# Performance work log

Hardware: AMD Instinct MI355X
Metric: run time of the kernel (lower is better)

The kernel has to match this reference:

```python
import jax, jax.numpy as jnp
import numpy as np

QDEPTH = 20
WIDTH = HEIGHT = 28
PIXELS = WIDTH * HEIGHT          # 784
WIRES = 10                        # ceil(log2(784))
BATCH = 8192


def setup_inputs() -> dict:
    key = jax.random.key(0)
    k1, k2, k3, k4 = jax.random.split(key, 4)
    x = jax.random.normal(k1, (BATCH, 1, WIDTH, HEIGHT), jnp.float32)
    W = jax.random.normal(k2, (WIRES, PIXELS), jnp.float32) / np.sqrt(PIXELS)
    b = jax.random.normal(k3, (WIRES,), jnp.float32) * 0.01
    qweights = jax.random.normal(k4, (QDEPTH, WIRES, 3), jnp.float32) * 0.4
    return {"x": x, "W": W, "b": b, "qweights": qweights}


def _apply_1q(state, gate, wire):
    """Apply a single-qubit gate. state: (B,)+(2,)*WIRES; gate: (2,2) or (B,2,2)."""
    ax = 1 + wire
    s = jnp.moveaxis(state, ax, 1)
    shp = s.shape
    s = s.reshape(shp[0], 2, -1)
    if gate.ndim == 2:
        s = jnp.einsum('ij,bjr->bir', gate, s)
    else:
        s = jnp.einsum('bij,bjr->bir', gate, s)
    return jnp.moveaxis(s.reshape(shp), 1, ax)


def _cnot(state, c, t):
    """CNOT with control c, target t on state (B,)+(2,)*WIRES."""
    s = jnp.moveaxis(state, (1 + c, 1 + t), (1, 2))
    # when control==1, flip target axis
    s = jnp.concatenate([s[:, :1], jnp.flip(s[:, 1:2], axis=2)], axis=1)
    return jnp.moveaxis(s, (1, 2), (1 + c, 1 + t))


def _ry_batched(theta):
    """theta: (B,) -> (B,2,2) complex RY gates."""
    c = jnp.cos(theta / 2)
    s = jnp.sin(theta / 2)
    g = jnp.stack([jnp.stack([c, -s], -1), jnp.stack([s, c], -1)], -2)
    return g.astype(jnp.complex64)


def _rot(phi, theta, omega):
    """PennyLane Rot(phi,theta,omega) = RZ(omega) RY(theta) RZ(phi), scalars -> (2,2)."""
    c = jnp.cos(theta / 2)
    s = jnp.sin(theta / 2)
    m00 = jnp.exp(-0.5j * (phi + omega)) * c
    m01 = -jnp.exp(0.5j * (phi - omega)) * s
    m10 = jnp.exp(-0.5j * (phi - omega)) * s
    m11 = jnp.exp(0.5j * (phi + omega)) * c
    return jnp.stack([jnp.stack([m00, m01]), jnp.stack([m10, m11])]).astype(jnp.complex64)


def _forward(x, W, b, qweights):
    B = x.shape[0]
    feat = x.reshape(B, -1)                       # b 1 w h -> b (w h)
    angles = feat @ W.T + b                       # linear_down -> (B, WIRES)

    # |0...0> statevector, wire 0 most significant (PennyLane convention)
    state = jnp.zeros((B,) + (2,) * WIRES, jnp.complex64)
    state = state.at[(slice(None),) + (0,) * WIRES].set(1.0)

    # AngleEmbedding, rotation='Y'
    for w in range(WIRES):
        state = _apply_1q(state, _ry_batched(angles[:, w]), w)

    # StronglyEntanglingLayers: per-layer Rot on every wire, then CNOT ring
    for l in range(QDEPTH):
        for w in range(WIRES):
            state = _apply_1q(state, _rot(qweights[l, w, 0], qweights[l, w, 1], qweights[l, w, 2]), w)
        r = (l % (WIRES - 1)) + 1                 # default PennyLane ranges
        for w in range(WIRES):
            state = _cnot(state, w, (w + r) % WIRES)

    sv = state.reshape(B, -1)
    probs = sv.real ** 2 + sv.imag ** 2           # qml.probs over all wires
    out = jnp.clip(probs[:, :PIXELS] * PIXELS, 0.0, 1.0)
    return out.reshape(B, 1, WIDTH, HEIGHT)


def reference(x, W, b, qweights):
    return _forward(x, W, b, qweights)
```

## Files before the change

kernel.cpp:

```cpp
#include <hip/hip_runtime.h>
#include <hip/hip_bf16.h>
#include <stdint.h>


#define NWIRES  10
#define DIM     1024
#define NLAYERS 20
#define NGATES  200
#define NPASS   100
#define PIXELS  784
#define BATCH   8192

typedef _Float16 f16;
typedef _Float16 f16x8 __attribute__((ext_vector_type(8)));
typedef float    f32x4 __attribute__((ext_vector_type(4)));
typedef float    f32x2 __attribute__((ext_vector_type(2)));

typedef const __attribute__((address_space(1))) void* gas1_t;
typedef __attribute__((address_space(3))) void*       las3_t;

__device__ __forceinline__ void gload_lds16(const void* g, void* l) {
  __builtin_amdgcn_global_load_lds((gas1_t)g, (las3_t)l, 16, 0, 0);
}

__global__ __launch_bounds__(256) void k_prep(const float* __restrict__ qw,
                                              float* __restrict__ plan_mat,
                                              unsigned* __restrict__ plan_idx,
                                              unsigned* __restrict__ plan_final,
                                              unsigned* __restrict__ jtab) {
  __shared__ float    gm[NGATES][8];
  __shared__ unsigned shb[NPASS * 8];
  __shared__ unsigned shr[NPASS * 8];
  __shared__ unsigned pp[NPASS][4];
  const int tid = threadIdx.x;

  if (tid < NGATES) {
    float phi = qw[tid * 3 + 0], th = qw[tid * 3 + 1], om = qw[tid * 3 + 2];
    float s, c, sa, ca, sb, cb;
    sincosf(0.5f * th, &s, &c);
    sincosf(0.5f * (phi + om), &sa, &ca);
    sincosf(0.5f * (phi - om), &sb, &cb);
    gm[tid][0] = ca * c;  gm[tid][1] = sa * c;
    gm[tid][2] = cb * s;  gm[tid][3] = sb * s;
    gm[tid][4] = -cb * s; gm[tid][5] = sb * s;
    gm[tid][6] = ca * c;  gm[tid][7] = -sa * c;
  }
  __syncthreads();

  if (tid == 0) {
    unsigned rA[NWIRES], ic[NWIRES];
#pragma unroll
    for (int i = 0; i < NWIRES; i++) { rA[i] = 1u << i; ic[i] = 1u << i; }
#pragma unroll
    for (int lrev = 0; lrev < NLAYERS; lrev++) {
      const int l = NLAYERS - 1 - lrev;
      const int r = (l % (NWIRES - 1)) + 1;
#pragma unroll
      for (int w = NWIRES - 1; w >= 0; w--) {
        const int t = (w + r) % NWIRES;
        rA[9 - t] ^= rA[9 - w];
        ic[9 - w] ^= ic[9 - t];
      }
#pragma unroll
      for (int s = 0; s < 5; s++) {
        const int p1 = 9 - 2 * s, p2 = 8 - 2 * s;
        unsigned u1 = rA[p1], u2 = rA[p2];
        unsigned m1 = ic[p1], m2 = ic[p2];
        unsigned b1 = u1 & (0u - u1);
        if (u2 & b1) u2 ^= u1;
        unsigned b2 = u2 & (0u - u2);
        if (u1 & b2) u1 ^= u2;
        const int pid = lrev * 5 + s;
        pp[pid][0] = u1; pp[pid][1] = u2;
        pp[pid][2] = b1; pp[pid][3] = b2;
        plan_idx[pid * 8 + 6] = m1;
        plan_idx[pid * 8 + 7] = m2;
      }
    }
#pragma unroll
    for (int p = 0; p < NWIRES; p++) plan_final[p] = ic[p];
  } else if (tid >= 100 && tid < 200) {
    int t = tid - 100;
    int lrev = t / 5, s = t % 5;
    int l = NLAYERS - 1 - lrev;
    int g1 = l * NWIRES + 2 * s, g2 = g1 + 1;
    float* K = plan_mat + (size_t)t * 64;
#pragma unroll
    for (int r = 0; r < 4; r++) {
#pragma unroll
      for (int c = 0; c < 4; c++) {
        int r1 = r >> 1, c1 = c >> 1, r2 = r & 1, c2 = c & 1;
        float ar = gm[g1][(r1 * 2 + c1) * 2], ai = gm[g1][(r1 * 2 + c1) * 2 + 1];
        float br = gm[g2][(r2 * 2 + c2) * 2], bi = gm[g2][(r2 * 2 + c2) * 2 + 1];
        float kr = ar * br - ai * bi;
        float ki = ar * bi + ai * br;
        float* e = K + (r * 4 + c) * 4;
        e[0] = kr; e[1] = kr; e[2] = -ki; e[3] = ki;
      }
    }
  }
  __syncthreads();

  if (tid < NPASS) {
    const int pid = tid;
    const unsigned u1 = pp[pid][0], u2 = pp[pid][1];
    const unsigned b1 = pp[pid][2], b2 = pp[pid][3];
    unsigned echPack = 0;
    int cnt = 0, nrem = 0;
    for (int f = 0; f < NWIRES; f++) {
      unsigned ef = 1u << f;
      if (ef == b1 || ef == b2) continue;
      unsigned v = ef ^ (((u1 >> f) & 1u) ? b1 : 0u)
                      ^ (((u2 >> f) & 1u) ? b2 : 0u);
      unsigned n = v & 15u;
#pragma unroll
      for (int rep = 0; rep < 4; rep++) {
#pragma unroll
        for (int k2 = 0; k2 < 4; k2++) {
          unsigned h = (echPack >> (8 * k2)) & 255u;
          if (h) {
            unsigned hb = 0x80000000u >> __clz(h);
            if (n & hb) n ^= h;
          }
        }
      }
      if (n && cnt < 4) {
        echPack |= n << (8 * cnt);
        shb[pid * 8 + cnt] = v;
        cnt++;
      } else {
        shr[pid * 8 + nrem] = v;
        nrem++;
      }
    }
    for (int i = 0; i < nrem; i++) shb[pid * 8 + cnt + i] = shr[pid * 8 + i];
  }
  __syncthreads();

  for (int t = 0; t < NPASS; t++) {
    unsigned j = 0;
#pragma unroll
    for (int b = 0; b < 8; b++)
      if ((tid >> b) & 1) j ^= shb[t * 8 + b];
    jtab[t * 256 + tid] = j;
  }
}

__global__ __launch_bounds__(256) void k_main(const float* __restrict__ plan_mat,
                                              const unsigned* __restrict__ plan_idx,
                                              const unsigned* __restrict__ plan_final,
                                              const unsigned* __restrict__ jtab,
                                              const float* __restrict__ x,
                                              const float* __restrict__ W,
                                              const float* __restrict__ bias,
                                              f16* __restrict__ E,
                                              f16* __restrict__ Bt) {
  __shared__ f32x2 st[DIM];
  __shared__ float part[4][NWIRES];
  __shared__ float csh[NWIRES][2];

  const int tid = threadIdx.x;

  if (blockIdx.x < PIXELS) {
    const int col = blockIdx.x;

    for (int i = tid; i < DIM; i += 256)
      st[i] = (f32x2){i == col ? 1.f : 0.f, 0.f};

    unsigned jn = jtab[tid];
    __syncthreads();

    for (int t = 0; t < NPASS; t++) {
      const unsigned* P = plan_idx + (size_t)t * 8;
      const unsigned m1 = P[6], m2 = P[7];
      const f32x4* Kp = (const f32x4*)(plan_mat + (size_t)t * 64);

      const unsigned j = jn;
      if (t + 1 < NPASS) jn = jtab[(t + 1) * 256 + tid];

      f32x2 v0 = st[j];
      f32x2 v1 = st[j ^ m2];
      f32x2 v2 = st[j ^ m1];
      f32x2 v3 = st[j ^ m1 ^ m2];
      f32x2 w0 = {v0.y, v0.x}, w1 = {v1.y, v1.x};
      f32x2 w2 = {v2.y, v2.x}, w3 = {v3.y, v3.x};

      f32x2 r0 = {0.f, 0.f}, r1 = {0.f, 0.f}, r2 = {0.f, 0.f}, r3 = {0.f, 0.f};
#define CM(rr, e, vv, ww)                         \
      { f32x4 kk = Kp[e];                         \
        rr += (f32x2){kk.x, kk.y} * (vv);         \
        rr += (f32x2){kk.z, kk.w} * (ww); }
      CM(r0, 0, v0, w0)  CM(r0, 1, v1, w1)  CM(r0, 2, v2, w2)  CM(r0, 3, v3, w3)
      CM(r1, 4, v0, w0)  CM(r1, 5, v1, w1)  CM(r1, 6, v2, w2)  CM(r1, 7, v3, w3)
      CM(r2, 8, v0, w0)  CM(r2, 9, v1, w1)  CM(r2, 10, v2, w2) CM(r2, 11, v3, w3)
      CM(r3, 12, v0, w0) CM(r3, 13, v1, w1) CM(r3, 14, v2, w2) CM(r3, 15, v3, w3)
#undef CM

      st[j]           = r0;
      st[j ^ m2]      = r1;
      st[j ^ m1]      = r2;
      st[j ^ m1 ^ m2] = r3;
      __syncthreads();
    }

    unsigned invl[NWIRES];
#pragma unroll
    for (int p = 0; p < NWIRES; p++) invl[p] = plan_final[p];

    __align__(8) f16 re4[4], im4[4];
#pragma unroll
    for (int u = 0; u < 4; u++) {
      int i = tid * 4 + u;
      unsigned j = 0;
#pragma unroll
      for (int p = 0; p < NWIRES; p++)
        if ((i >> p) & 1) j ^= invl[p];
      f32x2 v = st[j];
      re4[u] = (f16)v.x;
      im4[u] = (f16)(-v.y);
    }
    *(uint2*)(&Bt[(size_t)(2 * col) * DIM + tid * 4])     = *(const uint2*)re4;
    *(uint2*)(&Bt[(size_t)(2 * col + 1) * DIM + tid * 4]) = *(const uint2*)im4;
    return;
  }

  const int b = blockIdx.x - PIXELS;
  const float* xr = x + (size_t)b * PIXELS;

  float acc[NWIRES];
#pragma unroll
  for (int w = 0; w < NWIRES; w++) acc[w] = 0.f;

  for (int k = tid; k < PIXELS; k += 256) {
    float xv = xr[k];
#pragma unroll
    for (int w = 0; w < NWIRES; w++) acc[w] = fmaf(xv, W[w * PIXELS + k], acc[w]);
  }

#pragma unroll
  for (int w = 0; w < NWIRES; w++) {
    float v = acc[w];
#pragma unroll
    for (int off = 32; off > 0; off >>= 1) v += __shfl_xor(v, off, 64);
    acc[w] = v;
  }

  const int wv = tid >> 6, ln = tid & 63;
  if (ln == 0) {
#pragma unroll
    for (int w = 0; w < NWIRES; w++) part[wv][w] = acc[w];
  }
  __syncthreads();
  if (tid < NWIRES) {
    float a = part[0][tid] + part[1][tid] + part[2][tid] + part[3][tid] + bias[tid];
    float s, c;
    sincosf(0.5f * a, &s, &c);
    csh[tid][0] = c;
    csh[tid][1] = s;
  }
  __syncthreads();

  __align__(8) f16 e4[4];
#pragma unroll
  for (int u = 0; u < 4; u++) {
    int i = tid * 4 + u;
    float pr = 1.f;
#pragma unroll
    for (int w = 0; w < NWIRES; w++) pr *= csh[w][(i >> (9 - w)) & 1];
    e4[u] = (f16)pr;
  }
  *(uint2*)(&E[(size_t)b * DIM + tid * 4]) = *(const uint2*)e4;
}

__global__ __launch_bounds__(256, 2) void k_gemm(const f16* __restrict__ E,
                                                 const f16* __restrict__ Bt,
                                                 float* __restrict__ out) {
  __shared__ __align__(16) f16 As[4][128 * 32];
  __shared__ __align__(16) f16 Bs[4][128 * 32];

  const int tid = threadIdx.x;
  const int wid = tid >> 6, ln = tid & 63;
  const int wm = wid >> 1, wn = wid & 1;

  const int bid = blockIdx.x;
  const int swz = (bid & 7) * 104 + (bid >> 3);
  const int mt  = swz % 64, nt = swz / 64;
  const int m0  = mt * 128;
  const int n0  = nt * 128;

  f32x4 acc[4][4];
#pragma unroll
  for (int a = 0; a < 4; a++)
#pragma unroll
    for (int q = 0; q < 4; q++) acc[a][q] = (f32x4){0.f, 0.f, 0.f, 0.f};

  int offA[4], offB[4];
#pragma unroll
  for (int mi = 0; mi < 4; mi++) {
    int Ra = wm * 64 + mi * 16 + (ln & 15);
    offA[mi] = Ra * 32 + (((ln >> 4) ^ ((Ra >> 1) & 3)) * 8);
  }
#pragma unroll
  for (int ni = 0; ni < 4; ni++) {
    int Rb = wn * 64 + ni * 16 + (ln & 15);
    offB[ni] = Rb * 32 + (((ln >> 4) ^ ((Rb >> 1) & 3)) * 8);
  }

  auto stage = [&](int t) {
    const int sb = t & 3;
#pragma unroll
    for (int r = 0; r < 2; r++) {
      int u   = r * 256 + tid;
      int row = u >> 2;
      int c16 = (u & 3) ^ ((row >> 1) & 3);
      gload_lds16((const char*)E + (size_t)(m0 + row) * 2048 + t * 64 + c16 * 16,
                  (char*)&As[sb][0] + (size_t)u * 16);
    }
#pragma unroll
    for (int r = 0; r < 2; r++) {
      int u   = r * 256 + tid;
      int row = u >> 2;
      int c16 = (u & 3) ^ ((row >> 1) & 3);
      gload_lds16((const char*)Bt + (size_t)(n0 + row) * 2048 + t * 64 + c16 * 16,
                  (char*)&Bs[sb][0] + (size_t)u * 16);
    }
  };

  stage(0);
  stage(1);
  stage(2);
  asm volatile("s_waitcnt vmcnt(8)" ::: "memory");
  __builtin_amdgcn_s_barrier();

#pragma unroll 4
  for (int k = 0; k < 32; k++) {
    const int buf = k & 3;
    f16x8 af[4], bf[4];
#pragma unroll
    for (int mi = 0; mi < 4; mi++) af[mi] = *(const f16x8*)&As[buf][offA[mi]];
#pragma unroll
    for (int ni = 0; ni < 4; ni++) bf[ni] = *(const f16x8*)&Bs[buf][offB[ni]];

    if (k < 29) stage(k + 3);

    __builtin_amdgcn_s_setprio(1);
#pragma unroll
    for (int mi = 0; mi < 4; mi++)
#pragma unroll
      for (int ni = 0; ni < 4; ni++)
        acc[mi][ni] = __builtin_amdgcn_mfma_f32_16x16x32_f16(
            af[mi], bf[ni], acc[mi][ni], 0, 0, 0);
    __builtin_amdgcn_s_setprio(0);

    if (k < 29)       { asm volatile("s_waitcnt vmcnt(8)" ::: "memory"); }
    else if (k == 29) { asm volatile("s_waitcnt vmcnt(4)" ::: "memory"); }
    else if (k == 30) { asm volatile("s_waitcnt vmcnt(0)" ::: "memory"); }
    __builtin_amdgcn_s_barrier();
  }

#pragma unroll
  for (int mi = 0; mi < 4; mi++) {
#pragma unroll
    for (int ni = 0; ni < 4; ni++) {
      int n = n0 + wn * 64 + ni * 16 + (ln & 15);
      int p = n >> 1;
      bool even = (ln & 1) == 0;
#pragma unroll
      for (int r = 0; r < 4; r++) {
        float v = acc[mi][ni][r];
        float o = __shfl_xor(v, 1, 64);
        if (even && p < PIXELS) {
          int m = m0 + wm * 64 + mi * 16 + (ln >> 4) * 4 + r;
          float s2 = (v * v + o * o) * (float)PIXELS;
          out[(size_t)m * PIXELS + p] = fminf(fmaxf(s2, 0.f), 1.f);
        }
      }
    }
  }
}

extern "C" void kernel_launch(void* const* d_in, const int* in_sizes, int n_in,
                              void* d_out, int out_size, void* d_ws, size_t ws_size,
                              hipStream_t stream) {
  const float* x    = (const float*)d_in[0];
  const float* W    = (const float*)d_in[1];
  const float* bias = (const float*)d_in[2];
  const float* qw   = (const float*)d_in[3];
  float* out        = (float*)d_out;

  char* ws = (char*)d_ws;
  f16* E  = (f16*)(ws);
  f16* Bt = (f16*)(ws + (size_t)16 * 1024 * 1024);
  float*    plan_mat   = (float*)(ws + (size_t)20 * 1024 * 1024);
  unsigned* plan_idx   = (unsigned*)(ws + (size_t)20 * 1024 * 1024 + 65536);
  unsigned* plan_final = (unsigned*)(ws + (size_t)20 * 1024 * 1024 + 131072);
  unsigned* jtab       = (unsigned*)(ws + (size_t)20 * 1024 * 1024 + 196608);

  k_prep<<<dim3(1), dim3(256), 0, stream>>>(qw, plan_mat, plan_idx, plan_final,
                                            jtab);
  k_main<<<dim3(PIXELS + BATCH), dim3(256), 0, stream>>>(plan_mat, plan_idx,
                                                         plan_final, jtab,
                                                         x, W, bias, E, Bt);
  k_gemm<<<dim3(832), dim3(256), 0, stream>>>(E, Bt, out);
}
```

Baseline: 140.9 us.

## Enlarge GEMM tiles to 256x256 with 8 waves and quadrant-phased double buffering

The final GEMM moves from 128x128 tiles with 4 waves and a 4-deep K=32 pipeline to 256x256 tiles with 8 waves, K=64 steps and a double-buffered LDS split into four 128-row halves. Each K-tile is computed in four quadrant phases, and loads of the next halves are interleaved between phases, with an 8-way XOR swizzle for the wider rows. This raises arithmetic intensity and cuts global re-reads of E and Bt. The cost is a grid of only 224 blocks, which may leave the 256 CUs underfilled, plus 128 KB of LDS per block and higher register pressure.

```diff
diff --git a/kernel.cpp b/kernel.cpp
--- a/kernel.cpp
+++ b/kernel.cpp
@@ -272,105 +272,128 @@
   *(uint2*)(&E[(size_t)b * DIM + tid * 4]) = *(const uint2*)e4;
 }
 
-__global__ __launch_bounds__(256, 2) void k_gemm(const f16* __restrict__ E,
+__global__ __launch_bounds__(512, 2) void k_gemm(const f16* __restrict__ E,
                                                  const f16* __restrict__ Bt,
                                                  float* __restrict__ out) {
-  __shared__ __align__(16) f16 As[4][128 * 32];
-  __shared__ __align__(16) f16 Bs[4][128 * 32];
+  __shared__ __align__(16) f16 lds[8][128 * 64];
 
   const int tid = threadIdx.x;
   const int wid = tid >> 6, ln = tid & 63;
-  const int wm = wid >> 1, wn = wid & 1;
+  const int wm = wid >> 2, wn = wid & 3;
 
   const int bid = blockIdx.x;
-  const int swz = (bid & 7) * 104 + (bid >> 3);
-  const int mt  = swz % 64, nt = swz / 64;
-  const int m0  = mt * 128;
-  const int n0  = nt * 128;
-
-  f32x4 acc[4][4];
-#pragma unroll
-  for (int a = 0; a < 4; a++)
+  const int swz = (bid & 7) * 28 + (bid >> 3);
+  const int mt  = swz % 32, nt = swz / 32;
+  const int m0  = mt * 256;
+  const int n0  = nt * 256;
+
+  f32x4 acc[8][4];
+#pragma unroll
+  for (int a = 0; a < 8; a++)
 #pragma unroll
     for (int q = 0; q < 4; q++) acc[a][q] = (f32x4){0.f, 0.f, 0.f, 0.f};
 
-  int offA[4], offB[4];
-#pragma unroll
-  for (int mi = 0; mi < 4; mi++) {
-    int Ra = wm * 64 + mi * 16 + (ln & 15);
-    offA[mi] = Ra * 32 + (((ln >> 4) ^ ((Ra >> 1) & 3)) * 8);
-  }
-#pragma unroll
-  for (int ni = 0; ni < 4; ni++) {
-    int Rb = wn * 64 + ni * 16 + (ln & 15);
-    offB[ni] = Rb * 32 + (((ln >> 4) ^ ((Rb >> 1) & 3)) * 8);
-  }
-
-  auto stage = [&](int t) {
-    const int sb = t & 3;
-#pragma unroll
-    for (int r = 0; r < 2; r++) {
-      int u   = r * 256 + tid;
-      int row = u >> 2;
-      int c16 = (u & 3) ^ ((row >> 1) & 3);
-      gload_lds16((const char*)E + (size_t)(m0 + row) * 2048 + t * 64 + c16 * 16,
-                  (char*)&As[sb][0] + (size_t)u * 16);
-    }
-#pragma unroll
-    for (int r = 0; r < 2; r++) {
-      int u   = r * 256 + tid;
-      int row = u >> 2;
-      int c16 = (u & 3) ^ ((row >> 1) & 3);
-      gload_lds16((const char*)Bt + (size_t)(n0 + row) * 2048 + t * 64 + c16 * 16,
-                  (char*)&Bs[sb][0] + (size_t)u * 16);
+  int offA[4][2], offB[2][2];
+#pragma unroll
+  for (int mi = 0; mi < 4; mi++)
+#pragma unroll
+    for (int kk = 0; kk < 2; kk++) {
+      int r = (mi * 2 + wm) * 16 + (ln & 15);
+      offA[mi][kk] = r * 64 + (((kk * 4 + (ln >> 4)) ^ (r & 7)) * 8);
+    }
+#pragma unroll
+  for (int ni = 0; ni < 2; ni++)
+#pragma unroll
+    for (int kk = 0; kk < 2; kk++) {
+      int r = (ni * 4 + wn) * 16 + (ln & 15);
+      offB[ni][kk] = r * 64 + (((kk * 4 + (ln >> 4)) ^ (r & 7)) * 8);
+    }
+
+  auto stage = [&](int tile, int half_id) {
+    const int buf = tile & 1;
+    const f16* src = (half_id < 2) ? E : Bt;
+    const int rbase = ((half_id < 2) ? m0 : n0) + ((half_id & 1) ? 128 : 0);
+    f16* dst = &lds[buf * 4 + half_id][0];
+#pragma unroll
+    for (int r2 = 0; r2 < 2; r2++) {
+      int u   = r2 * 512 + tid;
+      int row = u >> 3;
+      int c8  = (u & 7) ^ (row & 7);
+      gload_lds16((const char*)src +
+                      ((size_t)(rbase + row) * 1024 + tile * 64 + c8 * 8) * 2,
+                  (char*)dst + (size_t)u * 16);
     }
   };
 
-  stage(0);
-  stage(1);
-  stage(2);
-  asm volatile("s_waitcnt vmcnt(8)" ::: "memory");
+#define PH(T, p)                                                              \
+  {                                                                           \
+    const int buf = (T) & 1;                                                  \
+    const int qm = (p) >> 1, qn = (p) & 1;                                    \
+    const f16* A_ = &lds[buf * 4 + qm][0];                                    \
+    const f16* B_ = &lds[buf * 4 + 2 + qn][0];                                \
+    f16x8 af[4][2], bf[2][2];                                                 \
+    _Pragma("unroll")                                                         \
+    for (int kk = 0; kk < 2; kk++) {                                          \
+      _Pragma("unroll")                                                       \
+      for (int mi = 0; mi < 4; mi++)                                          \
+        af[mi][kk] = *(const f16x8*)&A_[offA[mi][kk]];                        \
+      _Pragma("unroll")                                                       \
+      for (int ni = 0; ni < 2; ni++)                                          \
+        bf[ni][kk] = *(const f16x8*)&B_[offB[ni][kk]];                        \
+    }                                                                         \
+    if ((p) == 0)      { if ((T) <= 14) stage((T) + 1, 3); }                  \
+    else if ((p) == 1) { if ((T) <= 14) stage((T) + 1, 1); }                  \
+    else if ((p) == 2) { if ((T) <= 13) stage((T) + 2, 0); }                  \
+    else               { if ((T) <= 13) stage((T) + 2, 2); }                  \
+    __builtin_amdgcn_s_barrier();                                             \
+    asm volatile("s_waitcnt lgkmcnt(0)" ::: "memory");                        \
+    __builtin_amdgcn_s_setprio(1);                                            \
+    _Pragma("unroll")                                                         \
+    for (int kk = 0; kk < 2; kk++)                                            \
+      _Pragma("unroll")                                                       \
+      for (int mi = 0; mi < 4; mi++)                                          \
+        _Pragma("unroll")                                                     \
+        for (int ni = 0; ni < 2; ni++)                                        \
+          acc[qm * 4 + mi][qn * 2 + ni] =                                     \
+              __builtin_amdgcn_mfma_f32_16x16x32_f16(                         \
+                  af[mi][kk], bf[ni][kk], acc[qm * 4 + mi][qn * 2 + ni],      \
+                  0, 0, 0);                                                   \
+    __builtin_amdgcn_s_setprio(0);                                            \
+    if ((p) == 3) {                                                           \
+      if ((T) <= 13)      { asm volatile("s_waitcnt vmcnt(4)" ::: "memory"); }\
+      else if ((T) == 14) { asm volatile("s_waitcnt vmcnt(0)" ::: "memory"); }\
+    }                                                                         \
+    __builtin_amdgcn_s_barrier();                                             \
+  }
+
+  stage(0, 0); stage(0, 2); stage(0, 3); stage(0, 1);
+  stage(1, 0); stage(1, 2);
+  asm volatile("s_waitcnt vmcnt(4)" ::: "memory");
   __builtin_amdgcn_s_barrier();
 
-#pragma unroll 4
-  for (int k = 0; k < 32; k++) {
-    const int buf = k & 3;
-    f16x8 af[4], bf[4];
-#pragma unroll
-    for (int mi = 0; mi < 4; mi++) af[mi] = *(const f16x8*)&As[buf][offA[mi]];
-#pragma unroll
-    for (int ni = 0; ni < 4; ni++) bf[ni] = *(const f16x8*)&Bs[buf][offB[ni]];
-
-    if (k < 29) stage(k + 3);
-
-    __builtin_amdgcn_s_setprio(1);
-#pragma unroll
-    for (int mi = 0; mi < 4; mi++)
-#pragma unroll
-      for (int ni = 0; ni < 4; ni++)
-        acc[mi][ni] = __builtin_amdgcn_mfma_f32_16x16x32_f16(
-            af[mi], bf[ni], acc[mi][ni], 0, 0, 0);
-    __builtin_amdgcn_s_setprio(0);
-
-    if (k < 29)       { asm volatile("s_waitcnt vmcnt(8)" ::: "memory"); }
-    else if (k == 29) { asm volatile("s_waitcnt vmcnt(4)" ::: "memory"); }
-    else if (k == 30) { asm volatile("s_waitcnt vmcnt(0)" ::: "memory"); }
-    __builtin_amdgcn_s_barrier();
-  }
-
-#pragma unroll
-  for (int mi = 0; mi < 4; mi++) {
-#pragma unroll
-    for (int ni = 0; ni < 4; ni++) {
-      int n = n0 + wn * 64 + ni * 16 + (ln & 15);
-      int p = n >> 1;
+  for (int T = 0; T < 16; T++) {
+    PH(T, 0)
+    PH(T, 1)
+    PH(T, 2)
+    PH(T, 3)
+  }
+#undef PH
+
+#pragma unroll
+  for (int mig = 0; mig < 8; mig++) {
+#pragma unroll
+    for (int nig = 0; nig < 4; nig++) {
+      int gR = (mig >> 2) * 8 + (mig & 3) * 2 + wm;
+      int gC = (nig >> 1) * 8 + (nig & 1) * 4 + wn;
+      int n  = n0 + gC * 16 + (ln & 15);
+      int p  = n >> 1;
       bool even = (ln & 1) == 0;
 #pragma unroll
       for (int r = 0; r < 4; r++) {
-        float v = acc[mi][ni][r];
+        float v = acc[mig][nig][r];
         float o = __shfl_xor(v, 1, 64);
         if (even && p < PIXELS) {
-          int m = m0 + wm * 64 + mi * 16 + (ln >> 4) * 4 + r;
+          int m = m0 + gR * 16 + (ln >> 4) * 4 + r;
           float s2 = (v * v + o * o) * (float)PIXELS;
           out[(size_t)m * PIXELS + p] = fminf(fmaxf(s2, 0.f), 1.f);
         }
@@ -401,5 +424,5 @@
   k_main<<<dim3(PIXELS + BATCH), dim3(256), 0, stream>>>(plan_mat, plan_idx,
                                                          plan_final, jtab,
                                                          x, W, bias, E, Bt);
-  k_gemm<<<dim3(832), dim3(256), 0, stream>>>(E, Bt, out);
+  k_gemm<<<dim3(224), dim3(512), 0, stream>>>(E, Bt, out);
 }
```

Measured after the change: 130.7 us, median of 2. -7.2%, faster.
